# Kernel tuning notes

Hardware: AMD Instinct MI355X
Metric: run time of the kernel (lower is better)

The kernel has to match this reference:

```python
import jax, jax.numpy as jnp
import numpy as np

H = W = 64
C = 256
BZ = 4
EPS = 1e-8


def setup_inputs() -> dict:
    key = jax.random.key(0)
    k1, k2 = jax.random.split(key)
    inp = jax.random.normal(k1, (BZ, C, H, W), dtype=jnp.float32)
    ref = jax.random.normal(k2, (BZ, C, H, W), dtype=jnp.float32)
    # Central 32x32 hole in the 64x64 feature-space mask (raster-order indices,
    # matching util.cal_mask_given_mask_thred with shift_sz=1, stride=1, mask_thred=1).
    mask2d = np.zeros((H, W), dtype=np.int64)
    mask2d[16:48, 16:48] = 1
    flat = mask2d.reshape(-1)
    mask_idx = jnp.asarray(np.nonzero(flat == 1)[0], dtype=jnp.int32)    # M = 1024
    known_idx = jnp.asarray(np.nonzero(flat == 0)[0], dtype=jnp.int32)   # K = 3072
    return {"input": inp, "ref": ref, "mask_idx": mask_idx, "known_idx": known_idx}


def reference(input, ref, mask_idx, known_idx):
    bz, c, h, w = input.shape
    hw = h * w
    K = known_idx.shape[0]

    def one_image(inp, rf):
        inp_f = inp.reshape(c, hw)   # decoder features (patch source)
        rf_f = rf.reshape(c, hw)     # ref.relu4_3 features (match target)
        known = inp_f[:, known_idx]      # [c, K]  known 1x1 patches
        unknown = inp_f[:, mask_idx]     # [c, M]  unknown 1x1 patches
        kn = known / (jnp.linalg.norm(known, axis=0, keepdims=True) + EPS)
        un = unknown / (jnp.linalg.norm(unknown, axis=0, keepdims=True) + EPS)
        # conv_enc: cross-correlate ref features with L2-normalized known patches
        sim = jnp.einsum('ck,cp->pk', kn, rf_f)          # [hw, K]
        ind = jnp.argmax(sim, axis=1)                    # best known patch per pixel
        vmax = jnp.max(sim, axis=1)                      # its score
        vmax_m = vmax[mask_idx]                          # [M]
        best_ch = ind[mask_idx]                          # [M]
        best_known = known[:, best_ch].T                 # [M, c] known_region per mask pixel

        # Recurrent blend over masked pixels in raster order.
        # At t=0 the init (zeros) gives at=0 -> a_new=0, a_ori=1, reproducing the
        # ind_laten==0 branch (out=known_region, one-hot attention) exactly.
        def step(carry, xs):
            prev_out, prev_att = carry
            u_t, bk_t, vm_t, ch_t = xs
            at = jnp.dot(prev_out, u_t)
            denom = at + vm_t
            a_new = at / denom
            a_ori = vm_t / denom
            out = a_new * prev_out + a_ori * bk_t
            att = (prev_att * a_new).at[ch_t].add(a_ori)
            return (out, att), att

        init = (jnp.zeros((c,), inp.dtype), jnp.zeros((K,), inp.dtype))
        _, att_all = jax.lax.scan(step, init, (un.T, best_known, vmax_m, best_ch))

        # kbar: one-hot at known pixels, blended attention rows at masked pixels
        kbar = jax.nn.one_hot(ind, K, dtype=inp.dtype)   # [hw, K]
        kbar = kbar.at[mask_idx].set(att_all)
        # conv_new_dec: reconstruct from (non-normalized) known patches
        res = kbar @ known.T                             # [hw, c]
        return res.T.reshape(c, h, w)

    return jax.vmap(one_image)(input, ref)
```

## Files before the change

### kernel.cpp

```cpp
#include <hip/hip_runtime.h>
#include <hip/hip_bf16.h>
#include <math.h>

#define HWsz 4096
#define Csz  256
#define BZsz 4
#define Msz  1024
#define Ksz  3072
#define KSPL 6
#define KPER 512
#define NKT  4
#define LDP  132
#define KLD  140
#define MKSPL 8
#define MKPER 384
#define MNKT  3
#define MLDP  68

typedef float f32x2 __attribute__((ext_vector_type(2)));

#define PK_MUL(dst, s0, s1) asm("v_pk_mul_f32 %0, %1, %2" : "=v"(dst) : "v"(s0), "v"(s1))
#define PK_ADD(dst, s1)     asm("v_pk_add_f32 %0, %0, %1" : "+v"(dst) : "v"(s1))

__global__ void transpose_kernel(const float* __restrict__ in, float* __restrict__ outT) {
    __shared__ float tile[32][33];
    int b  = blockIdx.z;
    int p0 = blockIdx.x * 32;
    int c0 = blockIdx.y * 32;
    int tx = threadIdx.x;
    int ty = threadIdx.y;
#pragma unroll
    for (int i = 0; i < 4; i++) {
        int c = c0 + ty + i * 8;
        tile[ty + i * 8][tx] = in[((size_t)b * Csz + c) * HWsz + p0 + tx];
    }
    __syncthreads();
#pragma unroll
    for (int i = 0; i < 4; i++) {
        int p = p0 + ty + i * 8;
        outT[((size_t)b * HWsz + p) * Csz + c0 + tx] = tile[tx][ty + i * 8];
    }
}

__global__ void colnorm_kernel(const float* __restrict__ inp, float* __restrict__ dnorm) {
#pragma clang fp contract(off)
    int p = blockIdx.x * 256 + threadIdx.x;
    int b = blockIdx.y;
    const float* col = inp + (size_t)b * Csz * HWsz + p;
    float acc = 0.f;
    for (int c = 0; c < Csz; c++) {
        float x  = col[(size_t)c * HWsz];
        float sq = x * x;
        acc = acc + sq;
    }
    dnorm[b * HWsz + p] = sqrtf(acc) + 1e-8f;
}

__global__ void knprep_kernel(const float* __restrict__ inpT, const float* __restrict__ dnorm,
                              const int* __restrict__ kidx, float* __restrict__ knT) {
    int row  = blockIdx.x * 4 + (threadIdx.x >> 6);
    int lane = threadIdx.x & 63;
    int b    = blockIdx.y;
    int kid  = kidx[row];
    float dn = dnorm[b * HWsz + kid];
    const float* src = inpT + ((size_t)b * HWsz + kid) * Csz + lane * 4;
    float4 v = *(const float4*)src;
    float4 w = {v.x / dn, v.y / dn, v.z / dn, v.w / dn};
    *(float4*)(knT + ((size_t)b * Ksz + row) * Csz + lane * 4) = w;
}

__launch_bounds__(256, 2)
__global__ void masked_sim_kernel(const float* __restrict__ knT,
                                  const float* __restrict__ refm,
                                  const int* __restrict__ midx,
                                  float* __restrict__ pvmax, int* __restrict__ pind) {
#pragma clang fp contract(off)
    __shared__ float rf[64][MLDP];
    __shared__ float kn[64][KLD];

    int b   = blockIdx.x;
    int p0  = blockIdx.y * 64;
    int ks  = blockIdx.z;
    int k0  = ks * MKPER;
    int tid = threadIdx.x;

    int tr = tid >> 4;
    int tc = tid & 15;
    int kc = tc * 8 + ((tc >> 2) << 2);

    int skk  = tid >> 1;
    int sc4  = (tid & 1) * 32;
    int kcol = skk + ((skk >> 5) << 2);

    float best[4];
    int   bidx[4];
#pragma unroll
    for (int i = 0; i < 4; i++) { best[i] = -INFINITY; bidx[i] = 0x7fffffff; }

    for (int kt = 0; kt < MNKT; kt++) {
        int ktbase = k0 + kt * 128;
        const float* nrow = knT + ((size_t)b * Ksz + ktbase + skk) * Csz;

        f32x2 acc[4][4];
#pragma unroll
        for (int i = 0; i < 4; i++)
#pragma unroll
            for (int jj = 0; jj < 4; jj++) acc[i][jj] = (f32x2){0.f, 0.f};

        for (int cc = 0; cc < 4; cc++) {
            __syncthreads();
            {
                int pg  = (tid & 15) * 4;
                int pix = midx[p0 + pg];
#pragma unroll
                for (int i = 0; i < 4; i++) {
                    int c = i * 16 + (tid >> 4);
                    float4 v = *(const float4*)&refm[((size_t)b * Csz + cc * 64 + c) * HWsz + pix];
                    *(float4*)&rf[c][pg] = v;
                }
            }
            const float* src = nrow + cc * 64 + sc4;
#pragma unroll
            for (int i = 0; i < 8; i++) {
                float4 v = *(const float4*)(src + i * 4);
                int c = sc4 + i * 4;
                kn[c + 0][kcol] = v.x;
                kn[c + 1][kcol] = v.y;
                kn[c + 2][kcol] = v.z;
                kn[c + 3][kcol] = v.w;
            }
            __syncthreads();

#pragma unroll 2
            for (int c = 0; c < 64; c++) {
                float4 a0 = *(const float4*)&rf[c][tr * 4];
                float4 b0 = *(const float4*)&kn[c][kc];
                float4 b1 = *(const float4*)&kn[c][kc + 4];
                float av[4] = {a0.x, a0.y, a0.z, a0.w};
                f32x2 B[4] = {{b0.x, b0.y}, {b0.z, b0.w}, {b1.x, b1.y}, {b1.z, b1.w}};
#pragma unroll
                for (int i = 0; i < 4; i++) {
                    f32x2 av2 = {av[i], av[i]};
#pragma unroll
                    for (int jj = 0; jj < 4; jj++) {
                        f32x2 pr;
                        PK_MUL(pr, av2, B[jj]);
                        PK_ADD(acc[i][jj], pr);
                    }
                }
            }
        }
#pragma unroll
        for (int j = 0; j < 8; j++) {
            int k = ktbase + tc * 8 + j;
#pragma unroll
            for (int i = 0; i < 4; i++) {
                float v = (j & 1) ? acc[i][j >> 1].y : acc[i][j >> 1].x;
                if (v > best[i] || (v == best[i] && k < bidx[i])) { best[i] = v; bidx[i] = k; }
            }
        }
    }

    __syncthreads();
    float* sv = &rf[0][0];
    int*   si = (int*)&kn[0][0];
#pragma unroll
    for (int i = 0; i < 4; i++) {
        int p = tr * 4 + i;
        sv[p * 16 + tc] = best[i];
        si[p * 16 + tc] = bidx[i];
    }
    __syncthreads();
    if (tid < 64) {
        float bv = -INFINITY; int bi = 0x7fffffff;
        for (int t = 0; t < 16; t++) {
            float v = sv[tid * 16 + t];
            int   k = si[tid * 16 + t];
            if (v > bv || (v == bv && k < bi)) { bv = v; bi = k; }
        }
        int pix = midx[p0 + tid];
        pvmax[((size_t)ks * BZsz + b) * HWsz + pix] = bv;
        pind [((size_t)ks * BZsz + b) * HWsz + pix] = bi;
    }
}

__global__ void masked_combine_kernel(const float* __restrict__ pvmax, const int* __restrict__ pind,
                                      const int* __restrict__ midx,
                                      float* __restrict__ vmax, int* __restrict__ ind) {
    int i = blockIdx.x * 256 + threadIdx.x;
    int b = blockIdx.y;
    int pix = midx[i];
    float bv = -INFINITY; int bi = 0x7fffffff;
    for (int ks = 0; ks < MKSPL; ks++) {
        float v = pvmax[((size_t)ks * BZsz + b) * HWsz + pix];
        int   k = pind [((size_t)ks * BZsz + b) * HWsz + pix];
        if (v > bv || (v == bv && k < bi)) { bv = v; bi = k; }
    }
    vmax[b * HWsz + pix] = bv;
    ind [b * HWsz + pix] = bi;
}

__global__ void known_combine_kernel(const float* __restrict__ pvmax, const int* __restrict__ pind,
                                     const int* __restrict__ kidx,
                                     float* __restrict__ vmax, int* __restrict__ ind) {
    int i = blockIdx.x * 256 + threadIdx.x;
    int b = blockIdx.y;
    int pix = kidx[i];
    float bv = -INFINITY; int bi = 0x7fffffff;
    for (int ks = 0; ks < KSPL; ks++) {
        float v = pvmax[((size_t)ks * BZsz + b) * HWsz + pix];
        int   k = pind [((size_t)ks * BZsz + b) * HWsz + pix];
        if (v > bv || (v == bv && k < bi)) { bv = v; bi = k; }
    }
    vmax[b * HWsz + pix] = bv;
    ind [b * HWsz + pix] = bi;
}

__global__ void scanprep_kernel(const float* __restrict__ inpT, const float* __restrict__ dnorm,
                                const int* __restrict__ ind, const int* __restrict__ midx,
                                const int* __restrict__ kidx,
                                float* __restrict__ uT, float* __restrict__ bkT) {
    int t    = blockIdx.x * 4 + (threadIdx.x >> 6);
    int lane = threadIdx.x & 63;
    int b    = blockIdx.y;
    int pp   = midx[t];
    float dn = dnorm[b * HWsz + pp];
    int bkid = kidx[ind[b * HWsz + pp]];
    const float* us = inpT + ((size_t)b * HWsz + pp) * Csz + lane * 4;
    const float* bs = inpT + ((size_t)b * HWsz + bkid) * Csz + lane * 4;
    float4 v = *(const float4*)us;
    float4 w = {v.x / dn, v.y / dn, v.z / dn, v.w / dn};
    *(float4*)(uT  + ((size_t)b * Msz + t) * Csz + lane * 4) = w;
    *(float4*)(bkT + ((size_t)b * Msz + t) * Csz + lane * 4) = *(const float4*)bs;
}


#define CH(LQ4, RA_N, RB_N, RA_C, RB_C) \
    "v_readlane_b32 " #RA_N ", %[va], " #LQ4 "\n\t" \
    "v_add_f32 %[dot], " #RA_C ", %[dot]\n\t" \
    "v_readlane_b32 " #RB_N ", %[vb], " #LQ4 "\n\t" \
    "v_add_f32 %[dot], " #RB_C ", %[dot]\n\t"

#define CH_BLOCK8(L0, L1, L2, L3, L4, L5, L6, L7) \
    CH(L0, s44, s52, s40, s48) \
    CH(L1, s45, s53, s41, s49) \
    CH(L2, s46, s54, s42, s50) \
    CH(L3, s47, s55, s43, s51) \
    CH(L4, s40, s48, s44, s52) \
    CH(L5, s41, s49, s45, s53) \
    CH(L6, s42, s50, s46, s54) \
    CH(L7, s43, s51, s47, s55)

__launch_bounds__(256, 2)
__global__ void hetero_kernel(const float* __restrict__ knT, const float* __restrict__ refm,
                              const int* __restrict__ kidx,
                              float* __restrict__ pvmax, int* __restrict__ pind,
                              const float* __restrict__ uT, const float* __restrict__ bkT,
                              const float* __restrict__ vmax, const int* __restrict__ midx,
                              float* __restrict__ outT) {
#pragma clang fp contract(off)
    __shared__ float smem[17408];
    int gid = blockIdx.x;
    int tid = threadIdx.x;

    if (gid < BZsz) {
        float* L_vm = smem;
        int b = gid;
        for (int t = tid; t < Msz; t += 256) L_vm[t] = vmax[b * HWsz + midx[t]];
        __syncthreads();
        if (tid >= 64) return;
        __builtin_amdgcn_s_setprio(3);
        int lane = tid;

        const float* ub = uT  + (size_t)b * Msz * Csz + lane * 4;
        const float* bb = bkT + (size_t)b * Msz * Csz + lane * 4;
        float o0 = 0.f, o1 = 0.f, o2 = 0.f, o3 = 0.f;
        float4 Uc = *(const float4*)ub;
        float4 Bc = *(const float4*)bb;

        for (int t = 0; t < Msz; t++) {
            int tn = (t + 1) & (Msz - 1);
            float4 Un = *(const float4*)(ub + (size_t)tn * Csz);
            float4 Bn = *(const float4*)(bb + (size_t)tn * Csz);

            float pA = Uc.y * o1;
            float rA = __builtin_fmaf(Uc.x, o0, pA);
            float pB = Uc.w * o3;
            float rB = __builtin_fmaf(Uc.z, o2, pB);
            float dot = 0.f;
            asm volatile(
                "v_readlane_b32 s40, %[va], 0\n\t"
                "v_readlane_b32 s48, %[vb], 0\n\t"
                "v_readlane_b32 s41, %[va], 1\n\t"
                "v_readlane_b32 s49, %[vb], 1\n\t"
                "v_readlane_b32 s42, %[va], 2\n\t"
                "v_readlane_b32 s50, %[vb], 2\n\t"
                "v_readlane_b32 s43, %[va], 3\n\t"
                "v_readlane_b32 s51, %[vb], 3\n\t"
                CH_BLOCK8( 4,  5,  6,  7,  8,  9, 10, 11)
                CH_BLOCK8(12, 13, 14, 15, 16, 17, 18, 19)
                CH_BLOCK8(20, 21, 22, 23, 24, 25, 26, 27)
                CH_BLOCK8(28, 29, 30, 31, 32, 33, 34, 35)
                CH_BLOCK8(36, 37, 38, 39, 40, 41, 42, 43)
                CH_BLOCK8(44, 45, 46, 47, 48, 49, 50, 51)
                CH_BLOCK8(52, 53, 54, 55, 56, 57, 58, 59)
                CH(60, s44, s52, s40, s48)
                CH(61, s45, s53, s41, s49)
                CH(62, s46, s54, s42, s50)
                CH(63, s47, s55, s43, s51)
                "v_add_f32 %[dot], s44, %[dot]\n\t"
                "v_add_f32 %[dot], s52, %[dot]\n\t"
                "v_add_f32 %[dot], s45, %[dot]\n\t"
                "v_add_f32 %[dot], s53, %[dot]\n\t"
                "v_add_f32 %[dot], s46, %[dot]\n\t"
                "v_add_f32 %[dot], s54, %[dot]\n\t"
                "v_add_f32 %[dot], s47, %[dot]\n\t"
                "v_add_f32 %[dot], s55, %[dot]\n\t"
                : [dot] "+v"(dot)
                : [va] "v"(rA), [vb] "v"(rB)
                : "s40","s41","s42","s43","s44","s45","s46","s47",
                  "s48","s49","s50","s51","s52","s53","s54","s55");
            float at    = dot;
            float vm    = L_vm[t];
            float denom = at + vm;
            float anew  = at / denom;
            float aori  = vm / denom;
            float m0 = anew * o0, n0 = aori * Bc.x;
            float m1 = anew * o1, n1 = aori * Bc.y;
            float m2 = anew * o2, n2 = aori * Bc.z;
            float m3 = anew * o3, n3 = aori * Bc.w;
            o0 = m0 + n0; o1 = m1 + n1; o2 = m2 + n2; o3 = m3 + n3;
            float4 w = {o0, o1, o2, o3};
            *(float4*)&outT[((size_t)b * Msz + t) * Csz + lane * 4] = w;
            Uc = Un; Bc = Bn;
        }
        return;
    }

    int g  = gid - BZsz;
    int ks = g % KSPL;
    int pt = (g / KSPL) % 24;
    int b  = g / (24 * KSPL);
    int p0 = pt * 128;
    int k0 = ks * KPER;

    float (*rf)[LDP] = (float(*)[LDP])smem;
    float (*kn)[KLD] = (float(*)[KLD])(smem + 64 * LDP);

    int tr = tid >> 4;
    int tc = tid & 15;
    int kc = tc * 8 + ((tc >> 2) << 2);

    int rowgrp = tid >> 5;
    int px4    = (tid & 31) * 4;
    int skk  = tid >> 1;
    int sc4  = (tid & 1) * 32;
    int kcol = skk + ((skk >> 5) << 2);

    float best[8];
    int   bidx[8];
#pragma unroll
    for (int i = 0; i < 8; i++) { best[i] = -INFINITY; bidx[i] = 0x7fffffff; }

    for (int kt = 0; kt < NKT; kt++) {
        int ktbase = k0 + kt * 128;
        const float* nrow = knT + ((size_t)b * Ksz + ktbase + skk) * Csz;

        f32x2 acc[8][4];
#pragma unroll
        for (int i = 0; i < 8; i++)
#pragma unroll
            for (int jj = 0; jj < 4; jj++) acc[i][jj] = (f32x2){0.f, 0.f};

        for (int cc = 0; cc < 4; cc++) {
            __syncthreads();
            {
                int pix = kidx[p0 + px4];
#pragma unroll
                for (int i = 0; i < 8; i++) {
                    int c = i * 8 + rowgrp;
                    float4 v = *(const float4*)&refm[((size_t)b * Csz + cc * 64 + c) * HWsz + pix];
                    *(float4*)&rf[c][px4] = v;
                }
            }
            const float* src = nrow + cc * 64 + sc4;
#pragma unroll
            for (int i = 0; i < 8; i++) {
                float4 v = *(const float4*)(src + i * 4);
                int c = sc4 + i * 4;
                kn[c + 0][kcol] = v.x;
                kn[c + 1][kcol] = v.y;
                kn[c + 2][kcol] = v.z;
                kn[c + 3][kcol] = v.w;
            }
            __syncthreads();

#pragma unroll 2
            for (int c = 0; c < 64; c++) {
                float4 a0 = *(const float4*)&rf[c][tr * 8];
                float4 a1 = *(const float4*)&rf[c][tr * 8 + 4];
                float4 b0 = *(const float4*)&kn[c][kc];
                float4 b1 = *(const float4*)&kn[c][kc + 4];
                float av[8] = {a0.x, a0.y, a0.z, a0.w, a1.x, a1.y, a1.z, a1.w};
                f32x2 B[4] = {{b0.x, b0.y}, {b0.z, b0.w}, {b1.x, b1.y}, {b1.z, b1.w}};
#pragma unroll
                for (int i = 0; i < 8; i++) {
                    f32x2 av2 = {av[i], av[i]};
#pragma unroll
                    for (int jj = 0; jj < 4; jj++) {
                        f32x2 pr;
                        PK_MUL(pr, av2, B[jj]);
                        PK_ADD(acc[i][jj], pr);
                    }
                }
            }
        }
#pragma unroll
        for (int j = 0; j < 8; j++) {
            int k = ktbase + tc * 8 + j;
#pragma unroll
            for (int i = 0; i < 8; i++) {
                float v = (j & 1) ? acc[i][j >> 1].y : acc[i][j >> 1].x;
                if (v > best[i] || (v == best[i] && k < bidx[i])) { best[i] = v; bidx[i] = k; }
            }
        }
    }

    __syncthreads();
    float* sv = &rf[0][0];
    int*   si = (int*)&kn[0][0];
#pragma unroll
    for (int i = 0; i < 8; i++) {
        int p = tr * 8 + i;
        sv[p * 16 + tc] = best[i];
        si[p * 16 + tc] = bidx[i];
    }
    __syncthreads();
    if (tid < 128) {
        float bv = -INFINITY; int bi = 0x7fffffff;
        for (int t = 0; t < 16; t++) {
            float v = sv[tid * 16 + t];
            int   k = si[tid * 16 + t];
            if (v > bv || (v == bv && k < bi)) { bv = v; bi = k; }
        }
        int pix = kidx[p0 + tid];
        pvmax[((size_t)ks * BZsz + b) * HWsz + pix] = bv;
        pind [((size_t)ks * BZsz + b) * HWsz + pix] = bi;
    }
}

__global__ void maskpos_init(int* mp) { mp[blockIdx.x * 256 + threadIdx.x] = -1; }
__global__ void maskpos_set(const int* __restrict__ midx, int* mp) {
    int t = blockIdx.x * 256 + threadIdx.x;
    if (t < Msz) mp[midx[t]] = t;
}

#define FSTR 261
__launch_bounds__(256)
__global__ void finalize_kernel(const float* __restrict__ inpT, const float* __restrict__ outT,
                                const int* __restrict__ ind, const int* __restrict__ kidx,
                                const int* __restrict__ mp, float* __restrict__ out) {
    __shared__ float tile[64 * FSTR];
    int b   = blockIdx.x;
    int p0  = blockIdx.y * 64;
    int tid = threadIdx.x;
    int rl  = tid >> 6;
    int cc  = (tid & 63) * 4;
    for (int i = 0; i < 16; i++) {
        int r = rl + i * 4;
        int p = p0 + r;
        int m = mp[p];
        const float* src = (m >= 0) ? (outT + ((size_t)b * Msz + m) * Csz)
                                    : (inpT + ((size_t)b * HWsz + kidx[ind[b * HWsz + p]]) * Csz);
        float4 v = *(const float4*)(src + cc);
        tile[r * FSTR + cc + 0] = v.x;
        tile[r * FSTR + cc + 1] = v.y;
        tile[r * FSTR + cc + 2] = v.z;
        tile[r * FSTR + cc + 3] = v.w;
    }
    __syncthreads();
    int pp = tid & 63;
    int c0 = tid >> 6;
    for (int i = 0; i < 64; i++) {
        int c = c0 + i * 4;
        out[((size_t)b * Csz + c) * HWsz + p0 + pp] = tile[pp * FSTR + c];
    }
}

extern "C" void kernel_launch(void* const* d_in, const int* in_sizes, int n_in,
                              void* d_out, int out_size, void* d_ws, size_t ws_size,
                              hipStream_t stream) {
    const float* inp  = (const float*)d_in[0];
    const float* refm = (const float*)d_in[1];
    const int*   midx = (const int*)d_in[2];
    const int*   kidx = (const int*)d_in[3];
    float* out = (float*)d_out;

    char* ws = (char*)d_ws;
    float* inpT  = (float*)(ws);
    float* outT  = (float*)(ws + 16777216);
    float* knT   = (float*)(ws + 20971520);
    float* uT    = (float*)(ws + 33554432);
    float* bkT   = (float*)(ws + 37748736);
    float* dnorm = (float*)(ws + 41943040);
    float* vmax  = (float*)(ws + 42008576);
    int*   ind   = (int*)  (ws + 42074112);
    int*   mp    = (int*)  (ws + 42139648);
    float* pvmax = (float*)(ws + 42156032);
    int*   pind  = (int*)  (ws + 42680320);

    hipLaunchKernelGGL(transpose_kernel, dim3(HWsz / 32, Csz / 32, BZsz), dim3(32, 8), 0, stream,
                       inp, inpT);
    hipLaunchKernelGGL(maskpos_init, dim3(HWsz / 256), dim3(256), 0, stream, mp);
    hipLaunchKernelGGL(maskpos_set, dim3((Msz + 255) / 256), dim3(256), 0, stream, midx, mp);
    hipLaunchKernelGGL(colnorm_kernel, dim3(HWsz / 256, BZsz), dim3(256), 0, stream, inp, dnorm);
    hipLaunchKernelGGL(knprep_kernel, dim3(Ksz / 4, BZsz), dim3(256), 0, stream,
                       inpT, dnorm, kidx, knT);
    hipLaunchKernelGGL(masked_sim_kernel, dim3(BZsz, 16, MKSPL), dim3(256), 0, stream,
                       knT, refm, midx, pvmax, pind);
    hipLaunchKernelGGL(masked_combine_kernel, dim3(4, BZsz), dim3(256), 0, stream,
                       pvmax, pind, midx, vmax, ind);
    hipLaunchKernelGGL(scanprep_kernel, dim3(Msz / 4, BZsz), dim3(256), 0, stream,
                       inpT, dnorm, ind, midx, kidx, uT, bkT);
    hipLaunchKernelGGL(hetero_kernel, dim3(BZsz + BZsz * 24 * KSPL), dim3(256), 0, stream,
                       knT, refm, kidx, pvmax, pind, uT, bkT, vmax, midx, outT);
    hipLaunchKernelGGL(known_combine_kernel, dim3(Ksz / 256, BZsz), dim3(256), 0, stream,
                       pvmax, pind, kidx, vmax, ind);
    hipLaunchKernelGGL(finalize_kernel, dim3(BZsz, HWsz / 64), dim3(256), 0, stream,
                       inpT, outT, ind, kidx, mp, out);
}
```

Before: 942.1 us.

## Retile known-pixel similarity blocks to 256x128 with 512 threads and compact partials

```diff
diff --git a/kernel.cpp b/kernel.cpp
--- a/kernel.cpp
+++ b/kernel.cpp
@@ -7,15 +7,15 @@
 #define BZsz 4
 #define Msz  1024
 #define Ksz  3072
-#define KSPL 6
-#define KPER 512
-#define NKT  4
-#define LDP  132
+#define Knum 3072
+#define KSPL 24
+#define LDP  264
 #define KLD  140
 #define MKSPL 8
 #define MKPER 384
 #define MNKT  3
 #define MLDP  68
+#define MKLD  140
 
 typedef float f32x2 __attribute__((ext_vector_type(2)));
 
@@ -73,10 +73,10 @@
 __global__ void masked_sim_kernel(const float* __restrict__ knT,
                                   const float* __restrict__ refm,
                                   const int* __restrict__ midx,
-                                  float* __restrict__ pvmax, int* __restrict__ pind) {
+                                  float* __restrict__ mpv, int* __restrict__ mpi) {
 #pragma clang fp contract(off)
     __shared__ float rf[64][MLDP];
-    __shared__ float kn[64][KLD];
+    __shared__ float kn[64][MKLD];
 
     int b   = blockIdx.x;
     int p0  = blockIdx.y * 64;
@@ -178,40 +178,39 @@
             int   k = si[tid * 16 + t];
             if (v > bv || (v == bv && k < bi)) { bv = v; bi = k; }
         }
-        int pix = midx[p0 + tid];
-        pvmax[((size_t)ks * BZsz + b) * HWsz + pix] = bv;
-        pind [((size_t)ks * BZsz + b) * HWsz + pix] = bi;
-    }
-}
-
-__global__ void masked_combine_kernel(const float* __restrict__ pvmax, const int* __restrict__ pind,
+        mpv[((size_t)ks * BZsz + b) * Msz + p0 + tid] = bv;
+        mpi[((size_t)ks * BZsz + b) * Msz + p0 + tid] = bi;
+    }
+}
+
+__global__ void masked_combine_kernel(const float* __restrict__ mpv, const int* __restrict__ mpi,
                                       const int* __restrict__ midx,
                                       float* __restrict__ vmax, int* __restrict__ ind) {
     int i = blockIdx.x * 256 + threadIdx.x;
     int b = blockIdx.y;
-    int pix = midx[i];
     float bv = -INFINITY; int bi = 0x7fffffff;
     for (int ks = 0; ks < MKSPL; ks++) {
-        float v = pvmax[((size_t)ks * BZsz + b) * HWsz + pix];
-        int   k = pind [((size_t)ks * BZsz + b) * HWsz + pix];
+        float v = mpv[((size_t)ks * BZsz + b) * Msz + i];
+        int   k = mpi[((size_t)ks * BZsz + b) * Msz + i];
         if (v > bv || (v == bv && k < bi)) { bv = v; bi = k; }
     }
+    int pix = midx[i];
     vmax[b * HWsz + pix] = bv;
     ind [b * HWsz + pix] = bi;
 }
 
-__global__ void known_combine_kernel(const float* __restrict__ pvmax, const int* __restrict__ pind,
+__global__ void known_combine_kernel(const float* __restrict__ kpv, const int* __restrict__ kpi,
                                      const int* __restrict__ kidx,
                                      float* __restrict__ vmax, int* __restrict__ ind) {
     int i = blockIdx.x * 256 + threadIdx.x;
     int b = blockIdx.y;
-    int pix = kidx[i];
     float bv = -INFINITY; int bi = 0x7fffffff;
     for (int ks = 0; ks < KSPL; ks++) {
-        float v = pvmax[((size_t)ks * BZsz + b) * HWsz + pix];
-        int   k = pind [((size_t)ks * BZsz + b) * HWsz + pix];
+        float v = kpv[((size_t)ks * BZsz + b) * Knum + i];
+        int   k = kpi[((size_t)ks * BZsz + b) * Knum + i];
         if (v > bv || (v == bv && k < bi)) { bv = v; bi = k; }
     }
+    int pix = kidx[i];
     vmax[b * HWsz + pix] = bv;
     ind [b * HWsz + pix] = bi;
 }
@@ -251,22 +250,22 @@
     CH(L6, s42, s50, s46, s54) \
     CH(L7, s43, s51, s47, s55)
 
-__launch_bounds__(256, 2)
+__launch_bounds__(512, 1)
 __global__ void hetero_kernel(const float* __restrict__ knT, const float* __restrict__ refm,
                               const int* __restrict__ kidx,
-                              float* __restrict__ pvmax, int* __restrict__ pind,
+                              float* __restrict__ kpv, int* __restrict__ kpi,
                               const float* __restrict__ uT, const float* __restrict__ bkT,
                               const float* __restrict__ vmax, const int* __restrict__ midx,
                               float* __restrict__ outT) {
 #pragma clang fp contract(off)
-    __shared__ float smem[17408];
+    __shared__ float smem[64 * LDP + 64 * KLD];
     int gid = blockIdx.x;
     int tid = threadIdx.x;
 
     if (gid < BZsz) {
         float* L_vm = smem;
         int b = gid;
-        for (int t = tid; t < Msz; t += 256) L_vm[t] = vmax[b * HWsz + midx[t]];
+        for (int t = tid; t < Msz; t += 512) L_vm[t] = vmax[b * HWsz + midx[t]];
         __syncthreads();
         if (tid >= 64) return;
         __builtin_amdgcn_s_setprio(3);
@@ -339,22 +338,22 @@
 
     int g  = gid - BZsz;
     int ks = g % KSPL;
-    int pt = (g / KSPL) % 24;
-    int b  = g / (24 * KSPL);
-    int p0 = pt * 128;
-    int k0 = ks * KPER;
+    int pt = (g / KSPL) % 12;
+    int b  = g / (12 * KSPL);
+    int p0 = pt * 256;
+    int k0 = ks * 128;
 
     float (*rf)[LDP] = (float(*)[LDP])smem;
     float (*kn)[KLD] = (float(*)[KLD])(smem + 64 * LDP);
 
-    int tr = tid >> 4;
-    int tc = tid & 15;
-    int kc = tc * 8 + ((tc >> 2) << 2);
-
-    int rowgrp = tid >> 5;
-    int px4    = (tid & 31) * 4;
-    int skk  = tid >> 1;
-    int sc4  = (tid & 1) * 32;
+    int trp = tid >> 4;
+    int tc  = tid & 15;
+    int kc  = tc * 8 + ((tc >> 2) << 2);
+
+    int rowgrp = tid >> 6;
+    int px4    = (tid & 63) * 4;
+    int skk  = tid >> 2;
+    int sc4  = (tid & 3) * 16;
     int kcol = skk + ((skk >> 5) << 2);
 
     float best[8];
@@ -362,67 +361,64 @@
 #pragma unroll
     for (int i = 0; i < 8; i++) { best[i] = -INFINITY; bidx[i] = 0x7fffffff; }
 
-    for (int kt = 0; kt < NKT; kt++) {
-        int ktbase = k0 + kt * 128;
-        const float* nrow = knT + ((size_t)b * Ksz + ktbase + skk) * Csz;
-
-        f32x2 acc[8][4];
-#pragma unroll
-        for (int i = 0; i < 8; i++)
-#pragma unroll
-            for (int jj = 0; jj < 4; jj++) acc[i][jj] = (f32x2){0.f, 0.f};
-
-        for (int cc = 0; cc < 4; cc++) {
-            __syncthreads();
-            {
-                int pix = kidx[p0 + px4];
-#pragma unroll
-                for (int i = 0; i < 8; i++) {
-                    int c = i * 8 + rowgrp;
-                    float4 v = *(const float4*)&refm[((size_t)b * Csz + cc * 64 + c) * HWsz + pix];
-                    *(float4*)&rf[c][px4] = v;
+    const float* nrow = knT + ((size_t)b * Ksz + k0 + skk) * Csz;
+
+    f32x2 acc[8][4];
+#pragma unroll
+    for (int i = 0; i < 8; i++)
+#pragma unroll
+        for (int jj = 0; jj < 4; jj++) acc[i][jj] = (f32x2){0.f, 0.f};
+
+    for (int cc = 0; cc < 4; cc++) {
+        __syncthreads();
+        {
+            int pix = kidx[p0 + px4];
+#pragma unroll
+            for (int i = 0; i < 8; i++) {
+                int c = i * 8 + rowgrp;
+                float4 v = *(const float4*)&refm[((size_t)b * Csz + cc * 64 + c) * HWsz + pix];
+                *(float4*)&rf[c][px4] = v;
+            }
+        }
+        const float* src = nrow + cc * 64 + sc4;
+#pragma unroll
+        for (int i = 0; i < 4; i++) {
+            float4 v = *(const float4*)(src + i * 4);
+            int c = sc4 + i * 4;
+            kn[c + 0][kcol] = v.x;
+            kn[c + 1][kcol] = v.y;
+            kn[c + 2][kcol] = v.z;
+            kn[c + 3][kcol] = v.w;
+        }
+        __syncthreads();
+
+#pragma unroll 2
+        for (int c = 0; c < 64; c++) {
+            float4 a0 = *(const float4*)&rf[c][trp * 8];
+            float4 a1 = *(const float4*)&rf[c][trp * 8 + 4];
+            float4 b0 = *(const float4*)&kn[c][kc];
+            float4 b1 = *(const float4*)&kn[c][kc + 4];
+            float av[8] = {a0.x, a0.y, a0.z, a0.w, a1.x, a1.y, a1.z, a1.w};
+            f32x2 B[4] = {{b0.x, b0.y}, {b0.z, b0.w}, {b1.x, b1.y}, {b1.z, b1.w}};
+#pragma unroll
+            for (int i = 0; i < 8; i++) {
+                f32x2 av2 = {av[i], av[i]};
+#pragma unroll
+                for (int jj = 0; jj < 4; jj++) {
+                    f32x2 pr;
+                    PK_MUL(pr, av2, B[jj]);
+                    PK_ADD(acc[i][jj], pr);
                 }
             }
-            const float* src = nrow + cc * 64 + sc4;
-#pragma unroll
-            for (int i = 0; i < 8; i++) {
-                float4 v = *(const float4*)(src + i * 4);
-                int c = sc4 + i * 4;
-                kn[c + 0][kcol] = v.x;
-                kn[c + 1][kcol] = v.y;
-                kn[c + 2][kcol] = v.z;
-                kn[c + 3][kcol] = v.w;
-            }
-            __syncthreads();
-
-#pragma unroll 2
-            for (int c = 0; c < 64; c++) {
-                float4 a0 = *(const float4*)&rf[c][tr * 8];
-                float4 a1 = *(const float4*)&rf[c][tr * 8 + 4];
-                float4 b0 = *(const float4*)&kn[c][kc];
-                float4 b1 = *(const float4*)&kn[c][kc + 4];
-                float av[8] = {a0.x, a0.y, a0.z, a0.w, a1.x, a1.y, a1.z, a1.w};
-                f32x2 B[4] = {{b0.x, b0.y}, {b0.z, b0.w}, {b1.x, b1.y}, {b1.z, b1.w}};
-#pragma unroll
-                for (int i = 0; i < 8; i++) {
-                    f32x2 av2 = {av[i], av[i]};
-#pragma unroll
-                    for (int jj = 0; jj < 4; jj++) {
-                        f32x2 pr;
-                        PK_MUL(pr, av2, B[jj]);
-                        PK_ADD(acc[i][jj], pr);
-                    }
-                }
-            }
-        }
-#pragma unroll
-        for (int j = 0; j < 8; j++) {
-            int k = ktbase + tc * 8 + j;
-#pragma unroll
-            for (int i = 0; i < 8; i++) {
-                float v = (j & 1) ? acc[i][j >> 1].y : acc[i][j >> 1].x;
-                if (v > best[i] || (v == best[i] && k < bidx[i])) { best[i] = v; bidx[i] = k; }
-            }
+        }
+    }
+#pragma unroll
+    for (int j = 0; j < 8; j++) {
+        int k = k0 + tc * 8 + j;
+#pragma unroll
+        for (int i = 0; i < 8; i++) {
+            float v = (j & 1) ? acc[i][j >> 1].y : acc[i][j >> 1].x;
+            if (v > best[i] || (v == best[i] && k < bidx[i])) { best[i] = v; bidx[i] = k; }
         }
     }
 
@@ -431,21 +427,20 @@
     int*   si = (int*)&kn[0][0];
 #pragma unroll
     for (int i = 0; i < 8; i++) {
-        int p = tr * 8 + i;
+        int p = trp * 8 + i;
         sv[p * 16 + tc] = best[i];
         si[p * 16 + tc] = bidx[i];
     }
     __syncthreads();
-    if (tid < 128) {
+    if (tid < 256) {
         float bv = -INFINITY; int bi = 0x7fffffff;
         for (int t = 0; t < 16; t++) {
             float v = sv[tid * 16 + t];
             int   k = si[tid * 16 + t];
             if (v > bv || (v == bv && k < bi)) { bv = v; bi = k; }
         }
-        int pix = kidx[p0 + tid];
-        pvmax[((size_t)ks * BZsz + b) * HWsz + pix] = bv;
-        pind [((size_t)ks * BZsz + b) * HWsz + pix] = bi;
+        kpv[((size_t)ks * BZsz + b) * Knum + p0 + tid] = bv;
+        kpi[((size_t)ks * BZsz + b) * Knum + p0 + tid] = bi;
     }
 }
 
@@ -506,8 +501,10 @@
     float* vmax  = (float*)(ws + 42008576);
     int*   ind   = (int*)  (ws + 42074112);
     int*   mp    = (int*)  (ws + 42139648);
-    float* pvmax = (float*)(ws + 42156032);
-    int*   pind  = (int*)  (ws + 42680320);
+    float* mpv   = (float*)(ws + 42156032);
+    int*   mpi   = (int*)  (ws + 42287104);
+    float* kpv   = (float*)(ws + 42418176);
+    int*   kpi   = (int*)  (ws + 43597824);
 
     hipLaunchKernelGGL(transpose_kernel, dim3(HWsz / 32, Csz / 32, BZsz), dim3(32, 8), 0, stream,
                        inp, inpT);
@@ -517,15 +514,15 @@
     hipLaunchKernelGGL(knprep_kernel, dim3(Ksz / 4, BZsz), dim3(256), 0, stream,
                        inpT, dnorm, kidx, knT);
     hipLaunchKernelGGL(masked_sim_kernel, dim3(BZsz, 16, MKSPL), dim3(256), 0, stream,
-                       knT, refm, midx, pvmax, pind);
+                       knT, refm, midx, mpv, mpi);
     hipLaunchKernelGGL(masked_combine_kernel, dim3(4, BZsz), dim3(256), 0, stream,
-                       pvmax, pind, midx, vmax, ind);
+                       mpv, mpi, midx, vmax, ind);
     hipLaunchKernelGGL(scanprep_kernel, dim3(Msz / 4, BZsz), dim3(256), 0, stream,
                        inpT, dnorm, ind, midx, kidx, uT, bkT);
-    hipLaunchKernelGGL(hetero_kernel, dim3(BZsz + BZsz * 24 * KSPL), dim3(256), 0, stream,
-                       knT, refm, kidx, pvmax, pind, uT, bkT, vmax, midx, outT);
-    hipLaunchKernelGGL(known_combine_kernel, dim3(Ksz / 256, BZsz), dim3(256), 0, stream,
-                       pvmax, pind, kidx, vmax, ind);
+    hipLaunchKernelGGL(hetero_kernel, dim3(BZsz + BZsz * 12 * KSPL), dim3(512), 0, stream,
+                       knT, refm, kidx, kpv, kpi, uT, bkT, vmax, midx, outT);
+    hipLaunchKernelGGL(known_combine_kernel, dim3(Knum / 256, BZsz), dim3(256), 0, stream,
+                       kpv, kpi, kidx, vmax, ind);
     hipLaunchKernelGGL(finalize_kernel, dim3(BZsz, HWsz / 64), dim3(256), 0, stream,
                        inpT, outT, ind, kidx, mp, out);
 }
```

Result: faster. 780.2 us (-17.2%).
